# Performance work log

Hardware: AMD Instinct MI355X
Metric: run time of the kernel (lower is better)

The kernel has to match this reference:

```python
import jax, jax.numpy as jnp
import numpy as np

BI, BC = 128, 128      # image batch, caption batch
NR, NW = 36, 50        # regions per image, words per caption
EMB = 1024             # joint embedding dim
MASK = -1.0            # fill value for invalid (region, word) pairs


def setup_inputs() -> dict:
    key = jax.random.key(0)
    k1, k2, k3, k4 = jax.random.split(key, 4)
    imgs = jax.random.normal(k1, (BI, NR, EMB), dtype=jnp.float32)
    caps = jax.random.normal(k2, (BC, NW, EMB), dtype=jnp.float32)
    # valid lengths in [1, NR] / [1, NW]; force max so shapes are static
    img_lens = jax.random.randint(k3, (BI,), 1, NR + 1).at[0].set(NR).astype(jnp.int32)
    cap_lens = jax.random.randint(k4, (BC,), 1, NW + 1).at[0].set(NW).astype(jnp.int32)
    return {"imgs": imgs, "caps": caps, "img_lens": img_lens, "cap_lens": cap_lens}


def reference(imgs, caps, img_lens, cap_lens):
    # all-pairs region-word similarities: [bi, bc, n_r, n_w]
    n_r, n_w = imgs.shape[1], caps.shape[1]
    sims = jnp.einsum('ire,cwe->icrw', imgs, caps)
    # torch source computes sims under @torch.no_grad()
    sims = jax.lax.stop_gradient(sims)
    mask_i = jnp.arange(n_r) < img_lens[:, None]   # [bi, n_r]
    mask_c = jnp.arange(n_w) < cap_lens[:, None]   # [bc, n_w]
    mask = mask_i[:, None, :, None] & mask_c[None, :, None, :]  # [bi, bc, n_r, n_w]
    sims = jnp.where(mask, sims, MASK)
    # max-pool over region dim -> [bi, bc, n_w]
    return sims.max(axis=2)
```

## Files before the change

kernel.cpp:

```cpp
#include <hip/hip_runtime.h>
#include <cstdint>

#define NBI 128
#define NBC 128
#define NR_ 36
#define NW_ 50
#define EMB_ 1024
#define MTOT (NBI * NR_)
#define NTOT (NBC * NW_)
#define OUTN (NBI * NBC * NW_)

#define BM 144
#define MAXMB 44
#define ASLOTS (MAXMB * 144)
#define MT_NMB 0
#define MT_NNT 1
#define MT_NCOL 2
#define MT_IMGF 16
#define MT_LO 64
#define MT_ROWSRC 256
#define MT_COLSRC (256 + ASLOTS)
#define META_INTS (MT_COLSRC + NTOT)

typedef _Float16 f16;
typedef _Float16 f16x8 __attribute__((ext_vector_type(8)));
typedef float f32x4 __attribute__((ext_vector_type(4)));

__global__ void plan_kernel(const int* __restrict__ img_lens, const int* __restrict__ cap_lens,
                            int* __restrict__ meta) {
  __shared__ int s_imgf[45], s_lo[128], s_blk[128], s_capstart[128], s_scal[3];
  const int t = threadIdx.x;
  if (t == 0) {
    int nb = 0, used = 0;
    s_imgf[0] = 0;
    for (int i = 0; i < 128; ++i) {
      int len = img_lens[i];
      if (used + len > BM) { ++nb; s_imgf[nb] = i; used = 0; }
      s_blk[i] = nb; s_lo[i] = used; used += len;
    }
    ++nb; 
    for (int b = nb; b <= 44; ++b) s_imgf[b] = 128;
    s_scal[0] = nb;
    int nc = 0;
    for (int c = 0; c < 128; ++c) { s_capstart[c] = nc; nc += cap_lens[c]; }
    s_scal[1] = (nc + 127) >> 7;
    s_scal[2] = nc;
  }
  __syncthreads();
  if (t < 3) meta[MT_NMB + t] = s_scal[t];
  if (t < 45) meta[MT_IMGF + t] = s_imgf[t];
  if (t < 128) meta[MT_LO + t] = s_lo[t];
  for (int k = t; k < ASLOTS; k += 256) meta[MT_ROWSRC + k] = -1;
  for (int k = t; k < NTOT; k += 256) meta[MT_COLSRC + k] = -1;
  __syncthreads();
  if (t < 128) {
    int len = img_lens[t];
    int base = s_blk[t] * BM + s_lo[t];
    for (int r = 0; r < len; ++r) meta[MT_ROWSRC + base + r] = t * 36 + r;
    int cap = cap_lens[t];
    int cbase = s_capstart[t];
    for (int w = 0; w < cap; ++w) meta[MT_COLSRC + cbase + w] = t * 50 + w;
  }
}

__global__ void prep_kernel(const float* __restrict__ imgs, const float* __restrict__ caps,
                            const int* __restrict__ cap_lens, const int* __restrict__ meta,
                            f16* __restrict__ Af, f16* __restrict__ Bf, float* __restrict__ out) {
  int idx = blockIdx.x * 256 + threadIdx.x;
  const int nA = ASLOTS * 128;
  const int nB = NTOT * 128;
  if (idx < nA) {
    int row = idx >> 7, u = idx & 127;
    int src = meta[MT_ROWSRC + row];
    union { f16 h[8]; uint4 q; } r;
    if (src >= 0) {
      const float4* s = (const float4*)(imgs + (size_t)src * 1024 + u * 8);
      float4 a = s[0], b = s[1];
      r.h[0] = (f16)a.x; r.h[1] = (f16)a.y; r.h[2] = (f16)a.z; r.h[3] = (f16)a.w;
      r.h[4] = (f16)b.x; r.h[5] = (f16)b.y; r.h[6] = (f16)b.z; r.h[7] = (f16)b.w;
    } else {
      r.q = uint4{0u, 0u, 0u, 0u};
    }
    ((uint4*)Af)[idx] = r.q;
  } else if (idx < nA + nB) {
    int k = idx - nA;
    int row = k >> 7, u = k & 127;
    int src = meta[MT_COLSRC + row];
    union { f16 h[8]; uint4 q; } r;
    if (src >= 0) {
      const float4* s = (const float4*)(caps + (size_t)src * 1024 + u * 8);
      float4 a = s[0], b = s[1];
      r.h[0] = (f16)a.x; r.h[1] = (f16)a.y; r.h[2] = (f16)a.z; r.h[3] = (f16)a.w;
      r.h[4] = (f16)b.x; r.h[5] = (f16)b.y; r.h[6] = (f16)b.z; r.h[7] = (f16)b.w;
    } else {
      r.q = uint4{0u, 0u, 0u, 0u};
    }
    ((uint4*)Bf)[idx - nA] = r.q;
  } else {
    int k = idx - nA - nB;
    if (k < OUTN) {
      int col = k % 6400;
      int c = col / 50, w = col - 50 * c;
      if (w >= cap_lens[c]) out[k] = -1.0f;
    }
  }
}

__launch_bounds__(256, 3)
__global__ void gemm_max_kernel(const f16* __restrict__ A, const f16* __restrict__ B,
                                const int* __restrict__ img_lens,
                                const int* __restrict__ meta,
                                float* __restrict__ out) {
  __shared__ unsigned char smem[34816];

  const int bx = blockIdx.x;
  const int L = (bx & 7) * 275 + (bx >> 3);
  const int sc = L / 440;
  const int rem = L - sc * 440;
  const int bm = rem % 44;
  const int bn = sc * 10 + rem / 44;

  const int n_mblks = meta[MT_NMB];
  const int n_ntiles = meta[MT_NNT];
  if (bm >= n_mblks || bn >= n_ntiles) return;

  const int t = threadIdx.x;
  const int lane = t & 63;
  const int wv = t >> 6;

  f32x4 acc[9][2] = {};

  const char* Ab = (const char*)A + (size_t)(bm * BM) * 2048;
  const char* Bb = (const char*)B + (size_t)(bn * 128) * 2048;

  int sdstA[5], sgofA[5];
#pragma unroll
  for (int j = 0; j < 5; ++j) {
    int u = t + 256 * j;
    int row = u >> 3;
    int phys = (u & 7) * 16;
    int logical = phys ^ ((row & 7) << 4);
    sdstA[j] = u * 16;
    sgofA[j] = row * 2048 + logical;
  }
  int sdstB[4], sgofB[4];
#pragma unroll
  for (int j = 0; j < 4; ++j) {
    int u = t + 256 * j;
    int row = u >> 3;
    int phys = (u & 7) * 16;
    int logical = phys ^ ((row & 7) << 4);
    sdstB[j] = 18432 + u * 16;
    sgofB[j] = row * 2048 + logical;
  }

  for (int ck = 0; ck < 16; ++ck) {
    const int k0b = ck * 128;
#pragma unroll
    for (int j = 0; j < 4; ++j) {
      __builtin_amdgcn_global_load_lds(
          (const __attribute__((address_space(1))) void*)(Ab + (size_t)sgofA[j] + k0b),
          (__attribute__((address_space(3))) void*)(smem + sdstA[j]), 16, 0, 0);
    }
    if (t < 128) {
      __builtin_amdgcn_global_load_lds(
          (const __attribute__((address_space(1))) void*)(Ab + (size_t)sgofA[4] + k0b),
          (__attribute__((address_space(3))) void*)(smem + sdstA[4]), 16, 0, 0);
    }
#pragma unroll
    for (int j = 0; j < 4; ++j) {
      __builtin_amdgcn_global_load_lds(
          (const __attribute__((address_space(1))) void*)(Bb + (size_t)sgofB[j] + k0b),
          (__attribute__((address_space(3))) void*)(smem + sdstB[j]), 16, 0, 0);
    }
    __syncthreads();

#pragma unroll
    for (int kk = 0; kk < 2; ++kk) {
      f16x8 af[9], bf[2];
#pragma unroll
      for (int mt = 0; mt < 9; ++mt) {
        int row = mt * 16 + (lane & 15);
        int col = (kk * 64 + (lane >> 4) * 16) ^ ((row & 7) << 4);
        af[mt] = *(const f16x8*)(smem + row * 128 + col);
      }
#pragma unroll
      for (int nt = 0; nt < 2; ++nt) {
        int row = wv * 32 + nt * 16 + (lane & 15);
        int col = (kk * 64 + (lane >> 4) * 16) ^ ((row & 7) << 4);
        bf[nt] = *(const f16x8*)(smem + 18432 + row * 128 + col);
      }
#pragma unroll
      for (int mt = 0; mt < 9; ++mt)
#pragma unroll
        for (int nt = 0; nt < 2; ++nt)
          acc[mt][nt] = __builtin_amdgcn_mfma_f32_16x16x32_f16(af[mt], bf[nt], acc[mt][nt], 0, 0, 0);
    }
    __syncthreads();
  }

  const int q4 = ((lane >> 4) << 2);
  const int cg0 = bn * 128 + wv * 32 + (lane & 15);
  const int cg1 = cg0 + 16;
  int oc0 = -1, oc1 = -1;
  if (lane < 16) { oc0 = meta[MT_COLSRC + cg0]; oc1 = meta[MT_COLSRC + cg1]; }

  const int jf = meta[MT_IMGF + bm];
  const int jl = meta[MT_IMGF + bm + 1];
  for (int j = jf; j < jl; ++j) {
    const int len = img_lens[j];
    const int lo = meta[MT_LO + j];
    const int hi = lo + len;
    float v0 = -3.0e38f, v1 = -3.0e38f;
#pragma unroll
    for (int mt = 0; mt < 9; ++mt) {
#pragma unroll
      for (int r4 = 0; r4 < 4; ++r4) {
        int row = mt * 16 + q4 + r4;
        if (row >= lo && row < hi) {
          v0 = fmaxf(v0, acc[mt][0][r4]);
          v1 = fmaxf(v1, acc[mt][1][r4]);
        }
      }
    }
    v0 = fmaxf(v0, __shfl_xor(v0, 16)); v0 = fmaxf(v0, __shfl_xor(v0, 32));
    v1 = fmaxf(v1, __shfl_xor(v1, 16)); v1 = fmaxf(v1, __shfl_xor(v1, 32));
    if (len < NR_) { v0 = fmaxf(v0, -1.0f); v1 = fmaxf(v1, -1.0f); }
    if (lane < 16) {
      if (oc0 >= 0) out[(size_t)j * 6400 + oc0] = v0;
      if (oc1 >= 0) out[(size_t)j * 6400 + oc1] = v1;
    }
  }
}

extern "C" void kernel_launch(void* const* d_in, const int* in_sizes, int n_in,
                              void* d_out, int out_size, void* d_ws, size_t ws_size,
                              hipStream_t stream) {
  const float* imgs = (const float*)d_in[0];
  const float* caps = (const float*)d_in[1];
  const int* img_lens = (const int*)d_in[2];
  const int* cap_lens = (const int*)d_in[3];
  float* out = (float*)d_out;

  char* ws = (char*)d_ws;
  f16* Af = (f16*)ws;
  f16* Bf = (f16*)(ws + (size_t)ASLOTS * EMB_ * 2);
  int* meta = (int*)(ws + (size_t)ASLOTS * EMB_ * 2 + (size_t)NTOT * EMB_ * 2);

  const int nA = ASLOTS * 128;
  const int nB = NTOT * 128;
  const int nprep = nA + nB + OUTN;

  plan_kernel<<<1, 256, 0, stream>>>(img_lens, cap_lens, meta);
  prep_kernel<<<(nprep + 255) / 256, 256, 0, stream>>>(imgs, caps, cap_lens, meta, Af, Bf, out);
  gemm_max_kernel<<<MAXMB * 50, 256, 0, stream>>>(Af, Bf, img_lens, meta, out);
}
```

Measured before the change: 159.9 us.

## Double-buffer LDS K-chunks and compact active tile indices across XCDs

Switches the GEMM main loop to double-buffered LDS staging: the next K-chunk's global-to-LDS loads are issued before computing on the current buffer, cutting one barrier per iteration. LDS use doubles and launch bounds drop to 2 blocks per CU. The block index mapping now packs only active (bm, bn) tiles and spreads them evenly across the 8 XCDs, so idle blocks exit early without leaving gaps. Lower occupancy may reduce the latency hiding that multiple resident blocks provided.

```diff
diff --git a/kernel.cpp b/kernel.cpp
--- a/kernel.cpp
+++ b/kernel.cpp
@@ -20,7 +20,8 @@
 #define MT_LO 64
 #define MT_ROWSRC 256
 #define MT_COLSRC (256 + ASLOTS)
-#define META_INTS (MT_COLSRC + NTOT)
+
+#define LDSBUF 34816
 
 typedef _Float16 f16;
 typedef _Float16 f16x8 __attribute__((ext_vector_type(8)));
@@ -38,7 +39,7 @@
       if (used + len > BM) { ++nb; s_imgf[nb] = i; used = 0; }
       s_blk[i] = nb; s_lo[i] = used; used += len;
     }
-    ++nb; 
+    ++nb;
     for (int b = nb; b <= 44; ++b) s_imgf[b] = 128;
     s_scal[0] = nb;
     int nc = 0;
@@ -106,23 +107,69 @@
   }
 }
 
-__launch_bounds__(256, 3)
+#define STAGE(buf, ckk) do {                                                            \
+    const int sb_ = (buf) * LDSBUF;                                                     \
+    const int kb_ = (ckk) * 128;                                                        \
+    _Pragma("unroll")                                                                   \
+    for (int j = 0; j < 4; ++j)                                                         \
+      __builtin_amdgcn_global_load_lds(                                                 \
+          (const __attribute__((address_space(1))) void*)(Ab + (size_t)sgofA[j] + kb_), \
+          (__attribute__((address_space(3))) void*)(smem + sb_ + sdstA[j]), 16, 0, 0);  \
+    if (t < 128)                                                                        \
+      __builtin_amdgcn_global_load_lds(                                                 \
+          (const __attribute__((address_space(1))) void*)(Ab + (size_t)sgofA[4] + kb_), \
+          (__attribute__((address_space(3))) void*)(smem + sb_ + sdstA[4]), 16, 0, 0);  \
+    _Pragma("unroll")                                                                   \
+    for (int j = 0; j < 4; ++j)                                                         \
+      __builtin_amdgcn_global_load_lds(                                                 \
+          (const __attribute__((address_space(1))) void*)(Bb + (size_t)sgofB[j] + kb_), \
+          (__attribute__((address_space(3))) void*)(smem + sb_ + sdstB[j]), 16, 0, 0);  \
+  } while (0)
+
+#define COMPUTE(buf) do {                                                               \
+    const int sb_ = (buf) * LDSBUF;                                                     \
+    _Pragma("unroll")                                                                   \
+    for (int kk = 0; kk < 2; ++kk) {                                                    \
+      f16x8 af[9], bf[2];                                                               \
+      _Pragma("unroll")                                                                 \
+      for (int mt = 0; mt < 9; ++mt) {                                                  \
+        int row = mt * 16 + (lane & 15);                                                \
+        int col = (kk * 64 + (lane >> 4) * 16) ^ ((row & 7) << 4);                      \
+        af[mt] = *(const f16x8*)(smem + sb_ + row * 128 + col);                         \
+      }                                                                                 \
+      _Pragma("unroll")                                                                 \
+      for (int nt = 0; nt < 2; ++nt) {                                                  \
+        int row = wv * 32 + nt * 16 + (lane & 15);                                      \
+        int col = (kk * 64 + (lane >> 4) * 16) ^ ((row & 7) << 4);                      \
+        bf[nt] = *(const f16x8*)(smem + sb_ + 18432 + row * 128 + col);                 \
+      }                                                                                 \
+      _Pragma("unroll")                                                                 \
+      for (int mt = 0; mt < 9; ++mt)                                                    \
+        _Pragma("unroll")                                                               \
+        for (int nt = 0; nt < 2; ++nt)                                                  \
+          acc[mt][nt] = __builtin_amdgcn_mfma_f32_16x16x32_f16(af[mt], bf[nt],          \
+                                                               acc[mt][nt], 0, 0, 0);  \
+    }                                                                                   \
+  } while (0)
+
+__launch_bounds__(256, 2)
 __global__ void gemm_max_kernel(const f16* __restrict__ A, const f16* __restrict__ B,
                                 const int* __restrict__ img_lens,
                                 const int* __restrict__ meta,
                                 float* __restrict__ out) {
-  __shared__ unsigned char smem[34816];
-
-  const int bx = blockIdx.x;
-  const int L = (bx & 7) * 275 + (bx >> 3);
-  const int sc = L / 440;
-  const int rem = L - sc * 440;
-  const int bm = rem % 44;
-  const int bn = sc * 10 + rem / 44;
+  static __shared__ unsigned char smem[2 * LDSBUF];
 
   const int n_mblks = meta[MT_NMB];
   const int n_ntiles = meta[MT_NNT];
-  if (bm >= n_mblks || bn >= n_ntiles) return;
+  const int nact = n_mblks * n_ntiles;
+  const int bx = blockIdx.x;
+  if (bx >= nact) return;
+
+  const int xcd = bx & 7, idx = bx >> 3;
+  const int q = nact >> 3, r = nact & 7;
+  const int L = (xcd < r ? xcd * (q + 1) : r * (q + 1) + (xcd - r) * q) + idx;
+  const int bn = L / n_mblks;
+  const int bm = L - bn * n_mblks;
 
   const int t = threadIdx.x;
   const int lane = t & 63;
@@ -154,50 +201,14 @@
     sgofB[j] = row * 2048 + logical;
   }
 
-  for (int ck = 0; ck < 16; ++ck) {
-    const int k0b = ck * 128;
-#pragma unroll
-    for (int j = 0; j < 4; ++j) {
-      __builtin_amdgcn_global_load_lds(
-          (const __attribute__((address_space(1))) void*)(Ab + (size_t)sgofA[j] + k0b),
-          (__attribute__((address_space(3))) void*)(smem + sdstA[j]), 16, 0, 0);
-    }
-    if (t < 128) {
-      __builtin_amdgcn_global_load_lds(
-          (const __attribute__((address_space(1))) void*)(Ab + (size_t)sgofA[4] + k0b),
-          (__attribute__((address_space(3))) void*)(smem + sdstA[4]), 16, 0, 0);
-    }
-#pragma unroll
-    for (int j = 0; j < 4; ++j) {
-      __builtin_amdgcn_global_load_lds(
-          (const __attribute__((address_space(1))) void*)(Bb + (size_t)sgofB[j] + k0b),
-          (__attribute__((address_space(3))) void*)(smem + sdstB[j]), 16, 0, 0);
-    }
+  STAGE(0, 0);
+  __syncthreads();
+  for (int ck = 0; ck < 15; ++ck) {
+    STAGE((ck + 1) & 1, ck + 1);
+    COMPUTE(ck & 1);
     __syncthreads();
-
-#pragma unroll
-    for (int kk = 0; kk < 2; ++kk) {
-      f16x8 af[9], bf[2];
-#pragma unroll
-      for (int mt = 0; mt < 9; ++mt) {
-        int row = mt * 16 + (lane & 15);
-        int col = (kk * 64 + (lane >> 4) * 16) ^ ((row & 7) << 4);
-        af[mt] = *(const f16x8*)(smem + row * 128 + col);
-      }
-#pragma unroll
-      for (int nt = 0; nt < 2; ++nt) {
-        int row = wv * 32 + nt * 16 + (lane & 15);
-        int col = (kk * 64 + (lane >> 4) * 16) ^ ((row & 7) << 4);
-        bf[nt] = *(const f16x8*)(smem + 18432 + row * 128 + col);
-      }
-#pragma unroll
-      for (int mt = 0; mt < 9; ++mt)
-#pragma unroll
-        for (int nt = 0; nt < 2; ++nt)
-          acc[mt][nt] = __builtin_amdgcn_mfma_f32_16x16x32_f16(af[mt], bf[nt], acc[mt][nt], 0, 0, 0);
-    }
-    __syncthreads();
-  }
+  }
+  COMPUTE(1);
 
   const int q4 = ((lane >> 4) << 2);
   const int cg0 = bn * 128 + wv * 32 + (lane & 15);
```

New measurement: 141.8 us. 11.3% less time.
